# Performance work log

Measured on AMD Instinct MI355X. Metric: run time of the kernel, lower is better.

Reference implementation:

```python
import jax, jax.numpy as jnp
import numpy as np
from jax import lax

# Fixed dims from MSSMamba defaults
B_, L_, DM = 2, 8192, 256
NH, HP, NS = 4, 64, 8          # nheads, headdim, d_state
DIN = NH * HP                  # d_inner = 256
DPROJ = 2 * DIN + 2 * NS + NH  # 532


def setup_inputs() -> dict:
    key = jax.random.key(0)
    ks = jax.random.split(key, 16)
    f = lambda k, s, sc=1.0: jax.random.normal(k, s, jnp.float32) * sc
    inp = {
        'x_H': f(ks[0], (B_, L_, DM)),
        'x_V': f(ks[1], (B_, L_, DM)),
        'W_in_H': f(ks[2], (DM, 2 * DPROJ), 0.05),
        'W_in_V': f(ks[3], (DM, 2 * DPROJ), 0.05),
        'W_out_HF': f(ks[4], (DIN, DM), 0.05),
        'W_out_HB': f(ks[5], (DIN, DM), 0.05),
        'W_out_VF': f(ks[6], (DIN, DM), 0.05),
        'W_out_VB': f(ks[7], (DIN, DM), 0.05),
        'W_out': f(ks[8], (4 * DM, DM), 0.05),
    }
    for i, nm in enumerate(['HF', 'HB', 'VF', 'VB']):
        kd = jax.random.fold_in(ks[9], i)
        ka = jax.random.fold_in(ks[10], i)
        inp['dt_bias_' + nm] = f(kd, (NH,), 0.1)
        inp['A_log_' + nm] = jnp.log(jax.random.uniform(ka, (NH,), jnp.float32, 1.0, 16.0))
        inp['D_' + nm] = jnp.ones((NH,), jnp.float32)
    # per-batch permutation mapping vertical position -> horizontal position
    inp['v2h'] = jax.vmap(lambda k: jax.random.permutation(k, L_))(
        jax.random.split(ks[11], B_)).astype(jnp.int32)
    return inp


def _scan_dir(zxbcdt, dt_bias, A_log, D):
    # zxbcdt: [b, l, DPROJ] -> Mamba2-style selective scan, ngroups=1
    z = zxbcdt[..., :DIN].reshape(B_, L_, NH, HP)
    xBC = jax.nn.silu(zxbcdt[..., DIN:DIN + DIN + 2 * NS])
    x = xBC[..., :DIN].reshape(B_, L_, NH, HP)
    Bm = xBC[..., DIN:DIN + NS]      # [b, l, n]
    Cm = xBC[..., DIN + NS:]         # [b, l, n]
    dt = jax.nn.softplus(zxbcdt[..., -NH:] + dt_bias)  # [b, l, h]
    A = -jnp.exp(A_log)              # [h]
    dA = jnp.exp(dt * A)             # [b, l, h]
    dBx = jnp.einsum('blh,bln,blhp->blhpn', dt, Bm, x)  # [b,l,h,p,n]

    def step(state, inp):
        dA_t, dBx_t, C_t = inp
        state = dA_t[..., None, None] * state + dBx_t   # [b,h,p,n]
        y_t = jnp.einsum('bhpn,bn->bhp', state, C_t)
        return state, y_t

    init = jnp.zeros((B_, NH, HP, NS), dt.dtype)
    _, ys = lax.scan(step, init, (jnp.moveaxis(dA, 1, 0),
                                  jnp.moveaxis(dBx, 1, 0),
                                  jnp.moveaxis(Cm, 1, 0)))
    y = jnp.moveaxis(ys, 0, 1) + D[None, None, :, None] * x  # skip D*x
    y = y * jax.nn.silu(z)                                   # gate
    return y.reshape(B_, L_, DIN)


def reference(x_H, x_V, W_in_H, W_in_V,
              dt_bias_HF, dt_bias_HB, dt_bias_VF, dt_bias_VB,
              A_log_HF, A_log_HB, A_log_VF, A_log_VB,
              D_HF, D_HB, D_VF, D_VB,
              W_out_HF, W_out_HB, W_out_VF, W_out_VB,
              W_out, v2h):
    zx_HF, zx_HB = jnp.split(x_H @ W_in_H, 2, axis=-1)
    zx_VF, zx_VB = jnp.split(x_V @ W_in_V, 2, axis=-1)
    # note: source applies out_proj_HB to the HF branch (kept faithful)
    y_HF = _scan_dir(zx_HF, dt_bias_HF, A_log_HF, D_HF) @ W_out_HB
    y_HB = _scan_dir(zx_HB[:, ::-1], dt_bias_HB, A_log_HB, D_HB)[:, ::-1] @ W_out_HF
    y_VF = _scan_dir(zx_VF, dt_bias_VF, A_log_VF, D_VF) @ W_out_VB
    y_VB = _scan_dir(zx_VB[:, ::-1], dt_bias_VB, A_log_VB, D_VB)[:, ::-1] @ W_out_VF
    # remap vertical-ordered outputs to horizontal ordering (scatter by v2h)
    bidx = jnp.arange(B_)[:, None]
    y_VF = jnp.zeros_like(y_VF).at[bidx, v2h].set(y_VF)
    y_VB = jnp.zeros_like(y_VB).at[bidx, v2h].set(y_VB)
    cat = jnp.concatenate([y_HF, y_HB, y_VF, y_VB], axis=-1)  # [b, l, 4*d_model]
    return jax.nn.silu(cat) @ W_out
```

## Files before the change

kernel.cpp:

```cpp
#include <hip/hip_runtime.h>
#include <hip/hip_bf16.h>

#define B_N 2
#define L_N 8192
#define ROWS 16384
#define CHUNK 32
#define NCHUNK 256
#define GRP 16
#define NGRP 16
#define NPAD 1152

typedef __bf16 bf16x8 __attribute__((ext_vector_type(8)));
typedef float f32x4 __attribute__((ext_vector_type(4)));

__device__ __forceinline__ float siluf(float v) {
  return v * __builtin_amdgcn_rcpf(1.f + __expf(-v));
}
__device__ __forceinline__ float softplusf_(float v) {
  return fmaxf(v, 0.f) + log1pf(__expf(-fabsf(v)));
}
__device__ __forceinline__ unsigned short f2bf(float v) {
  union { __bf16 b; unsigned short u; } x;
  x.b = (__bf16)v;
  return x.u;
}
__device__ __forceinline__ float bf2f(unsigned short u) {
  union { unsigned u; float f; } x; x.u = ((unsigned)u) << 16;
  return x.f;
}

__device__ __forceinline__ void gload_lds16(const unsigned short* g, unsigned short* l) {
  __builtin_amdgcn_global_load_lds(
      (const __attribute__((address_space(1))) unsigned int*)g,
      (__attribute__((address_space(3))) unsigned int*)l, 16, 0, 0);
}

struct P4 { const float* p[4]; };
struct ScanConsts {
  const float* dt_bias[4];
  const float* A_log[4];
  const float* D[4];
};

__global__ __launch_bounds__(256) void k_prep(
    const float* __restrict__ xH, const float* __restrict__ xV,
    const float* __restrict__ WH, const float* __restrict__ WV,
    P4 ws, const float* __restrict__ W_out, const int* __restrict__ v2h, ScanConsts sc,
    unsigned short* __restrict__ xbf, float* __restrict__ dtv_arr, float* __restrict__ dA_arr,
    unsigned short* __restrict__ Wt_in, unsigned short* __restrict__ Wt_dirs,
    unsigned short* __restrict__ Wt_fin, int* __restrict__ inv) {
  __shared__ float xs[32][257];
  __shared__ float Wsm[8][260];
  int bid = blockIdx.x;
  int tid = threadIdx.x;
  if (bid < 1024) {
    const int mat = bid >> 9;
    const float* x = mat ? xV : xH;
    const float* W = mat ? WV : WH;
    const int r0 = (bid & 511) * 32;
    for (int i = tid; i < 2048; i += 256) {
      int c = i >> 8, k = i & 255;
      int sl = c >> 2, h = c & 3;
      Wsm[c][k] = W[(long)k * 1064 + sl * 532 + 528 + h];
    }
    for (int i = tid; i < 32 * 64; i += 256) {
      int rl = i >> 6, kq = (i & 63) * 4;
      float4 v = *(const float4*)(x + (long)(r0 + rl) * 256 + kq);
      xs[rl][kq + 0] = v.x; xs[rl][kq + 1] = v.y; xs[rl][kq + 2] = v.z; xs[rl][kq + 3] = v.w;
    }
    __syncthreads();
    for (int i = tid; i < 32 * 64; i += 256) {
      int rl = i >> 6, kq = (i & 63) * 4;
      ushort4 o;
      o.x = f2bf(xs[rl][kq + 0]);
      o.y = f2bf(xs[rl][kq + 1]);
      o.z = f2bf(xs[rl][kq + 2]);
      o.w = f2bf(xs[rl][kq + 3]);
      *(ushort4*)(xbf + (size_t)mat * ROWS * 256 + (long)(r0 + rl) * 256 + kq) = o;
    }
    const int rl = tid >> 3, c = tid & 7;
    float s = 0.f;
    #pragma unroll 8
    for (int k = 0; k < 256; ++k) s = fmaf(xs[rl][k], Wsm[c][k], s);
    const int sl = c >> 2, h = c & 3;
    const int dir = mat * 2 + sl;
    float dtv = softplusf_(s + sc.dt_bias[dir][h]);
    float dAv = __expf(dtv * (-__expf(sc.A_log[dir][h])));
    long o = ((long)dir * 4 + h) * ROWS + (r0 + rl);
    dtv_arr[o] = dtv;
    dA_arr[o] = dAv;
  } else if (bid < 3328) {
    int i = (bid - 1024) * 256 + tid;
    int z = i / (NPAD * 256);
    int rem = i - z * (NPAD * 256);
    int n = rem >> 8, k = rem & 255;
    const float* W = z ? WV : WH;
    int sl = n >= 544;
    int cc = n - (sl ? 544 : 0);
    float v = (cc < 532) ? W[(long)k * 1064 + sl * 532 + cc] : 0.f;
    Wt_in[i] = f2bf(v);
  } else if (bid < 4352) {
    int i = (bid - 3328) * 256 + tid;
    int d = i >> 16;
    int rem = i & 65535;
    int n = rem >> 8, k = rem & 255;
    Wt_dirs[i] = f2bf(ws.p[d][(long)k * 256 + n]);
  } else if (bid < 5376) {
    int i = (bid - 4352) * 256 + tid;
    int n = i >> 10, k = i & 1023;
    Wt_fin[i] = f2bf(W_out[(long)k * 256 + n]);
  } else {
    int m = (bid - 5376) * 256 + tid;
    if (m < ROWS) {
      int b = m >> 13;
      inv[b * L_N + v2h[m]] = m;
    }
  }
}

struct EpiIn {
  unsigned short* zraw;
  unsigned short* xraw;
  unsigned short* bc;
};

__global__ __launch_bounds__(256) void k_gemm_in(
    const unsigned short* __restrict__ Abase, const unsigned short* __restrict__ Btbase,
    EpiIn ep) {
  __shared__ unsigned short smem[16384];
  unsigned short* AsB = smem;
  unsigned short* BsB = smem + 8192;
  const int tid = threadIdx.x;
  const int lane = tid & 63;
  const int wid = tid >> 6;
  const int wm = wid & 1, wn = wid >> 1;
  const int q = lane >> 4, r = lane & 15;
  const int m0 = blockIdx.x * 128;
  const int n0 = blockIdx.y * 128;
  const int z = blockIdx.z;
  const unsigned short* A = Abase + (long)z * ROWS * 256;
  const unsigned short* Bt = Btbase + (long)z * NPAD * 256;

  int s_row[2], s_ch[2];
  #pragma unroll
  for (int i = 0; i < 2; ++i) {
    int idx = i * 256 + tid;
    s_row[i] = idx >> 2;
    s_ch[i] = (idx & 3) ^ ((s_row[i] >> 1) & 3);
  }

  f32x4 acc[4][4] = {};
  const int swr = (r >> 1) & 3;
  int cur = 0;

  #pragma unroll
  for (int i = 0; i < 2; ++i) {
    gload_lds16(A + (long)(m0 + s_row[i]) * 256 + s_ch[i] * 8,
                AsB + (size_t)(i * 256 + wid * 64) * 8);
    gload_lds16(Bt + (long)(n0 + s_row[i]) * 256 + s_ch[i] * 8,
                BsB + (size_t)(i * 256 + wid * 64) * 8);
  }
  __syncthreads();

  for (int kt8 = 0; kt8 < 8; ++kt8) {
    const int kt = kt8 * 32;
    if (kt8 < 7) {
      #pragma unroll
      for (int i = 0; i < 2; ++i) {
        gload_lds16(A + (long)(m0 + s_row[i]) * 256 + kt + 32 + s_ch[i] * 8,
                    AsB + (size_t)((cur ^ 1) * 4096 + (i * 256 + wid * 64) * 8));
        gload_lds16(Bt + (long)(n0 + s_row[i]) * 256 + kt + 32 + s_ch[i] * 8,
                    BsB + (size_t)((cur ^ 1) * 4096 + (i * 256 + wid * 64) * 8));
      }
    }
    bf16x8 af[4], bfr[4];
    #pragma unroll
    for (int mi = 0; mi < 4; ++mi)
      af[mi] = *(const bf16x8*)&AsB[cur * 4096 + ((wm * 64 + mi * 16 + r) * 4 + (q ^ swr)) * 8];
    #pragma unroll
    for (int ni = 0; ni < 4; ++ni)
      bfr[ni] = *(const bf16x8*)&BsB[cur * 4096 + ((wn * 64 + ni * 16 + r) * 4 + (q ^ swr)) * 8];
    __builtin_amdgcn_s_setprio(1);
    #pragma unroll
    for (int mi = 0; mi < 4; ++mi)
      #pragma unroll
      for (int ni = 0; ni < 4; ++ni)
        acc[mi][ni] = __builtin_amdgcn_mfma_f32_16x16x32_bf16(af[mi], bfr[ni], acc[mi][ni], 0, 0, 0);
    __builtin_amdgcn_s_setprio(0);
    __syncthreads();
    cur ^= 1;
  }

  unsigned short* tr = smem + wid * (16 * 72);
  #pragma unroll
  for (int mi = 0; mi < 4; ++mi) {
    #pragma unroll
    for (int ni = 0; ni < 4; ++ni)
      #pragma unroll
      for (int j = 0; j < 4; ++j)
        tr[(q * 4 + j) * 72 + ni * 16 + r] = f2bf(acc[mi][ni][j]);
    asm volatile("s_waitcnt lgkmcnt(0)" ::: "memory");
    #pragma unroll
    for (int pass = 0; pass < 2; ++pass) {
      int rl = pass * 8 + (lane >> 3);
      int c8 = (lane & 7) * 8;
      bf16x8 v = *(const bf16x8*)&tr[rl * 72 + c8];
      int row = m0 + wm * 64 + mi * 16 + rl;
      int col = n0 + wn * 64 + c8;
      int sl = col >= 544;
      int cc = col - (sl ? 544 : 0);
      if (cc < 528) {
        int dir = z * 2 + sl;
        if (cc < 256)
          *(bf16x8*)(ep.zraw + ((long)dir * ROWS + row) * 256 + cc) = v;
        else if (cc < 512)
          *(bf16x8*)(ep.xraw + ((long)dir * ROWS + row) * 256 + cc - 256) = v;
        else
          *(bf16x8*)(ep.bc + ((long)dir * ROWS + row) * 16 + cc - 512) = v;
      }
    }
    asm volatile("s_waitcnt lgkmcnt(0)" ::: "memory");
  }
}

__global__ __launch_bounds__(512, 4) void k_fuse(
    const unsigned short* __restrict__ ybf,
    const unsigned short* __restrict__ Wt_dirs,
    const unsigned short* __restrict__ Wt_fin,
    unsigned short* __restrict__ pbuf) {
  __shared__ unsigned short Ab[2][64 * 32];
  __shared__ unsigned short Bb[2][256 * 32];
  __shared__ unsigned short Tl[64 * 264];
  const int tid = threadIdx.x;
  const int lane = tid & 63;
  const int wid = tid >> 6;
  const int wm = wid & 1, wn = wid >> 1;
  const int q = lane >> 4, r = lane & 15;
  const int r0 = blockIdx.x * 64;
  const int pair = blockIdx.y;
  const int swr = (r >> 1) & 3;

  const int a_row = tid >> 2;
  const int a_ch = (tid & 3) ^ ((a_row >> 1) & 3);
  const long a_off = (long)(r0 + a_row) * 256 + a_ch * 8;
  int b_row[2], b_ch[2];
  #pragma unroll
  for (int rnd = 0; rnd < 2; ++rnd) {
    int idx = rnd * 512 + tid;
    b_row[rnd] = idx >> 2;
    b_ch[rnd] = (idx & 3) ^ ((b_row[rnd] >> 1) & 3);
  }

  f32x4 acc_o[2][4] = {};
  int cur = 0;

  {
    const unsigned short* yd = ybf + (long)(pair * 2) * ROWS * 256;
    const unsigned short* Wd = Wt_dirs + (long)(pair * 2) * 65536;
    if (tid < 256)
      gload_lds16(yd + a_off, &Ab[0][(size_t)(wid * 64) * 8]);
    #pragma unroll
    for (int rnd = 0; rnd < 2; ++rnd)
      gload_lds16(Wd + (long)b_row[rnd] * 256 + b_ch[rnd] * 8,
                  &Bb[0][(size_t)(rnd * 512 + wid * 64) * 8]);
  }
  __syncthreads();

  #pragma unroll
  for (int dd = 0; dd < 2; ++dd) {
    const int d = pair * 2 + dd;
    const unsigned short* yd = ybf + (long)d * ROWS * 256;
    const unsigned short* Wd = Wt_dirs + (long)d * 65536;

    f32x4 acc_t[2][4] = {};
    for (int kt8 = 0; kt8 < 8; ++kt8) {
      const int kt = kt8 * 32;
      if (kt8 < 7) {
        if (tid < 256)
          gload_lds16(yd + a_off + kt + 32, &Ab[cur ^ 1][(size_t)(wid * 64) * 8]);
        #pragma unroll
        for (int rnd = 0; rnd < 2; ++rnd)
          gload_lds16(Wd + (long)b_row[rnd] * 256 + kt + 32 + b_ch[rnd] * 8,
                      &Bb[cur ^ 1][(size_t)(rnd * 512 + wid * 64) * 8]);
      } else {
        #pragma unroll
        for (int rnd = 0; rnd < 2; ++rnd)
          gload_lds16(Wt_fin + (long)b_row[rnd] * 1024 + d * 256 + b_ch[rnd] * 8,
                      &Bb[cur ^ 1][(size_t)(rnd * 512 + wid * 64) * 8]);
      }
      bf16x8 af[2], bfr[4];
      #pragma unroll
      for (int mi = 0; mi < 2; ++mi)
        af[mi] = *(const bf16x8*)&Ab[cur][((wm * 32 + mi * 16 + r) * 4 + (q ^ swr)) * 8];
      #pragma unroll
      for (int ni = 0; ni < 4; ++ni)
        bfr[ni] = *(const bf16x8*)&Bb[cur][((wn * 64 + ni * 16 + r) * 4 + (q ^ swr)) * 8];
      __builtin_amdgcn_s_setprio(1);
      #pragma unroll
      for (int mi = 0; mi < 2; ++mi)
        #pragma unroll
        for (int ni = 0; ni < 4; ++ni)
          acc_t[mi][ni] = __builtin_amdgcn_mfma_f32_16x16x32_bf16(af[mi], bfr[ni], acc_t[mi][ni], 0, 0, 0);
      __builtin_amdgcn_s_setprio(0);
      __syncthreads();
      cur ^= 1;
    }
    #pragma unroll
    for (int mi = 0; mi < 2; ++mi)
      #pragma unroll
      for (int ni = 0; ni < 4; ++ni)
        #pragma unroll
        for (int j = 0; j < 4; ++j)
          Tl[(wm * 32 + mi * 16 + q * 4 + j) * 264 + wn * 64 + ni * 16 + r] =
              f2bf(siluf(acc_t[mi][ni][j]));
    __syncthreads();
    for (int kt8 = 0; kt8 < 8; ++kt8) {
      const int kt = kt8 * 32;
      if (kt8 < 7) {
        #pragma unroll
        for (int rnd = 0; rnd < 2; ++rnd)
          gload_lds16(Wt_fin + (long)b_row[rnd] * 1024 + d * 256 + kt + 32 + b_ch[rnd] * 8,
                      &Bb[cur ^ 1][(size_t)(rnd * 512 + wid * 64) * 8]);
      } else if (dd == 0) {
        const unsigned short* yd1 = ybf + (long)(d + 1) * ROWS * 256;
        const unsigned short* Wd1 = Wt_dirs + (long)(d + 1) * 65536;
        if (tid < 256)
          gload_lds16(yd1 + a_off, &Ab[cur ^ 1][(size_t)(wid * 64) * 8]);
        #pragma unroll
        for (int rnd = 0; rnd < 2; ++rnd)
          gload_lds16(Wd1 + (long)b_row[rnd] * 256 + b_ch[rnd] * 8,
                      &Bb[cur ^ 1][(size_t)(rnd * 512 + wid * 64) * 8]);
      }
      bf16x8 af[2], bfr[4];
      #pragma unroll
      for (int mi = 0; mi < 2; ++mi)
        af[mi] = *(const bf16x8*)&Tl[(wm * 32 + mi * 16 + r) * 264 + kt + q * 8];
      #pragma unroll
      for (int ni = 0; ni < 4; ++ni)
        bfr[ni] = *(const bf16x8*)&Bb[cur][((wn * 64 + ni * 16 + r) * 4 + (q ^ swr)) * 8];
      __builtin_amdgcn_s_setprio(1);
      #pragma unroll
      for (int mi = 0; mi < 2; ++mi)
        #pragma unroll
        for (int ni = 0; ni < 4; ++ni)
          acc_o[mi][ni] = __builtin_amdgcn_mfma_f32_16x16x32_bf16(af[mi], bfr[ni], acc_o[mi][ni], 0, 0, 0);
      __builtin_amdgcn_s_setprio(0);
      __syncthreads();
      cur ^= 1;
    }
  }

  #pragma unroll
  for (int mi = 0; mi < 2; ++mi)
    #pragma unroll
    for (int ni = 0; ni < 4; ++ni)
      #pragma unroll
      for (int j = 0; j < 4; ++j)
        Tl[(wm * 32 + mi * 16 + q * 4 + j) * 264 + wn * 64 + ni * 16 + r] = f2bf(acc_o[mi][ni][j]);
  __syncthreads();
  unsigned short* pout = pbuf + (long)pair * ROWS * 256;
  #pragma unroll
  for (int pass = 0; pass < 4; ++pass) {
    int id = pass * 512 + tid;
    int row = id >> 5, c8 = (id & 31) * 8;
    bf16x8 v = *(const bf16x8*)&Tl[row * 264 + c8];
    *(bf16x8*)(pout + (long)(r0 + row) * 256 + c8) = v;
  }
}

__global__ void k_red(const unsigned short* __restrict__ pbuf,
                      const int* __restrict__ inv, float* __restrict__ out) {
  int i = blockIdx.x * 256 + threadIdx.x;
  int row = i >> 5, c8 = (i & 31) * 8;
  uint4 a = *(const uint4*)(pbuf + (long)row * 256 + c8);
  int vrow = inv[row];
  uint4 b = *(const uint4*)(pbuf + (size_t)ROWS * 256 + (long)vrow * 256 + c8);
  const unsigned short* au = (const unsigned short*)&a;
  const unsigned short* bu = (const unsigned short*)&b;
  float rr[8];
  #pragma unroll
  for (int j = 0; j < 8; ++j) rr[j] = bf2f(au[j]) + bf2f(bu[j]);
  ((float4*)out)[i * 2] = *(float4*)&rr[0];
  ((float4*)out)[i * 2 + 1] = *(float4*)&rr[4];
}

struct ScanP {
  const unsigned short* xraw;
  const unsigned short* zraw;
  const unsigned short* bc;
  const float* dtv;
  const float* dA;
  const float* D[4];
};

__global__ __launch_bounds__(64) void k_scan1(ScanP sp, float* __restrict__ S,
                                              float* __restrict__ P) {
  __shared__ __align__(16) float Bst[CHUNK][8];
  __shared__ float dAs[CHUNK];
  const int p = threadIdx.x;
  const int c = blockIdx.x;
  const int bh = blockIdx.y;
  const int d = blockIdx.z;
  const int b = bh >> 2, h = bh & 3;
  const int rev = d & 1;
  const int t0 = c * CHUNK;
  if (p < CHUNK) {
    const int t = t0 + p;
    const int l = rev ? (L_N - 1 - t) : t;
    const int row = (b << 13) + l;
    uint4 bv = *(const uint4*)(sp.bc + ((long)d * ROWS + row) * 16);
    const unsigned short* bu = (const unsigned short*)&bv;
    float dtvv = sp.dtv[((long)d * 4 + h) * ROWS + row];
    dAs[p] = sp.dA[((long)d * 4 + h) * ROWS + row];
    #pragma unroll
    for (int n = 0; n < 8; ++n) Bst[p][n] = siluf(bf2f(bu[n])) * dtvv;
  }
  __syncthreads();

  float st[8] = {0, 0, 0, 0, 0, 0, 0, 0};
  float cumdA = 1.f;
  const int l0 = rev ? (L_N - 1 - t0) : t0;
  const unsigned short* xp = sp.xraw + ((long)d * ROWS + (b << 13) + l0) * 256 + h * 64 + p;
  const long stp = rev ? -256L : 256L;

  unsigned short xa[8], xb[8];
  #pragma unroll
  for (int j = 0; j < 8; ++j) xa[j] = xp[(long)j * stp];
  #pragma unroll
  for (int g = 0; g < 4; ++g) {
    if (g < 3) {
      #pragma unroll
      for (int j = 0; j < 8; ++j) xb[j] = xp[(long)((g + 1) * 8 + j) * stp];
    }
    #pragma unroll
    for (int j = 0; j < 8; ++j) {
      int s = g * 8 + j;
      float x = siluf(bf2f(xa[j]));
      float dA = dAs[s];
      f32x4 B0 = *(const f32x4*)&Bst[s][0];
      f32x4 B1 = *(const f32x4*)&Bst[s][4];
      cumdA *= dA;
      st[0] = fmaf(dA, st[0], x * B0[0]);
      st[1] = fmaf(dA, st[1], x * B0[1]);
      st[2] = fmaf(dA, st[2], x * B0[2]);
      st[3] = fmaf(dA, st[3], x * B0[3]);
      st[4] = fmaf(dA, st[4], x * B1[0]);
      st[5] = fmaf(dA, st[5], x * B1[1]);
      st[6] = fmaf(dA, st[6], x * B1[2]);
      st[7] = fmaf(dA, st[7], x * B1[3]);
    }
    #pragma unroll
    for (int j = 0; j < 8; ++j) xa[j] = xb[j];
  }
  float* Sp = S + ((((long)d * NCHUNK + c) * 8 + bh) * 64 + p) * 8;
  #pragma unroll
  for (int n = 0; n < 8; ++n) Sp[n] = st[n];
  if (p == 0) P[((long)d * NCHUNK + c) * 8 + bh] = cumdA;
}

__global__ __launch_bounds__(512) void k_scan2a(const float* __restrict__ S,
                                                const float* __restrict__ P,
                                                float* __restrict__ carry_loc,
                                                float* __restrict__ Sg,
                                                float* __restrict__ Pg) {
  __shared__ float Pl[GRP];
  const int tid = threadIdx.x;
  const int gid = blockIdx.x;
  const int g = gid & 15;
  const int dbh = gid >> 4;
  const int d = dbh >> 3, bh = dbh & 7;
  if (tid < GRP) Pl[tid] = P[((long)d * NCHUNK + g * GRP + tid) * 8 + bh];
  __syncthreads();
  float cy = 0.f;
  #pragma unroll
  for (int i = 0; i < GRP; ++i) {
    const int c = g * GRP + i;
    carry_loc[(((long)d * NCHUNK + c) * 8 + bh) * 512 + tid] = cy;
    const float Sv = S[(((long)d * NCHUNK + c) * 8 + bh) * 512 + tid];
    cy = fmaf(Pl[i], cy, Sv);
  }
  Sg[(((long)d * NGRP + g) * 8 + bh) * 512 + tid] = cy;
  if (tid == 0) {
    float pp = 1.f;
    #pragma unroll
    for (int i = 0; i < GRP; ++i) pp *= Pl[i];
    Pg[((long)d * NGRP + g) * 8 + bh] = pp;
  }
}

__global__ __launch_bounds__(512) void k_scan2b(const float* __restrict__ Sg,
                                                const float* __restrict__ Pg,
                                                float* __restrict__ gcarry) {
  __shared__ float Pgl[NGRP];
  const int tid = threadIdx.x;
  const int dbh = blockIdx.x;
  const int d = dbh >> 3, bh = dbh & 7;
  if (tid < NGRP) Pgl[tid] = Pg[((long)d * NGRP + tid) * 8 + bh];
  __syncthreads();
  float cy = 0.f;
  #pragma unroll
  for (int g = 0; g < NGRP; ++g) {
    gcarry[(((long)d * NGRP + g) * 8 + bh) * 512 + tid] = cy;
    const float Sv = Sg[(((long)d * NGRP + g) * 8 + bh) * 512 + tid];
    cy = fmaf(Pgl[g], cy, Sv);
  }
}

__global__ __launch_bounds__(64) void k_scan3(ScanP sp,
                                              const float* __restrict__ carry_loc,
                                              const float* __restrict__ gcarry,
                                              const float* __restrict__ Pc,
                                              unsigned short* __restrict__ ybf) {
  __shared__ __align__(16) float Bst[CHUNK][8];
  __shared__ __align__(16) float Cst[CHUNK][8];
  __shared__ float dAs[CHUNK];
  __shared__ float Pgr[GRP];
  const int p = threadIdx.x;
  const int c = blockIdx.x;
  const int bh = blockIdx.y;
  const int d = blockIdx.z;
  const int b = bh >> 2, h = bh & 3;
  const int rev = d & 1;
  const float Dv = sp.D[d][h];
  const int t0 = c * CHUNK;
  const int grp = c >> 4, ii = c & 15;
  if (p < ii) Pgr[p] = Pc[((long)d * NCHUNK + grp * GRP + p) * 8 + bh];
  if (p < CHUNK) {
    const int t = t0 + p;
    const int l = rev ? (L_N - 1 - t) : t;
    const int row = (b << 13) + l;
    const unsigned short* bp = sp.bc + ((long)d * ROWS + row) * 16;
    uint4 bv = *(const uint4*)bp;
    uint4 cv = *(const uint4*)(bp + 8);
    const unsigned short* bu = (const unsigned short*)&bv;
    const unsigned short* cu = (const unsigned short*)&cv;
    float dtvv = sp.dtv[((long)d * 4 + h) * ROWS + row];
    dAs[p] = sp.dA[((long)d * 4 + h) * ROWS + row];
    #pragma unroll
    for (int n = 0; n < 8; ++n) Bst[p][n] = siluf(bf2f(bu[n])) * dtvv;
    #pragma unroll
    for (int n = 0; n < 8; ++n) Cst[p][n] = siluf(bf2f(cu[n]));
  }
  __syncthreads();

  float pref = 1.f;
  for (int k = 0; k < ii; ++k) pref *= Pgr[k];
  float st[8];
  {
    const float* clp = carry_loc + ((((long)d * NCHUNK + c) * 8 + bh) * 64 + p) * 8;
    const float* gcp = gcarry + ((((long)d * NGRP + grp) * 8 + bh) * 64 + p) * 8;
    #pragma unroll
    for (int n = 0; n < 8; ++n) st[n] = fmaf(pref, gcp[n], clp[n]);
  }

  const int l0 = rev ? (L_N - 1 - t0) : t0;
  const long base = (long)(b << 13) + l0;
  const unsigned short* xp = sp.xraw + ((long)d * ROWS + base) * 256 + h * 64 + p;
  const unsigned short* zp = sp.zraw + ((long)d * ROWS + base) * 256 + h * 64 + p;
  unsigned short* yp = ybf + ((long)d * ROWS + base) * 256 + h * 64 + p;
  const long stp = rev ? -256L : 256L;

  unsigned short xa[8], xb[8], za[8], zb[8];
  #pragma unroll
  for (int j = 0; j < 8; ++j) { xa[j] = xp[(long)j * stp]; za[j] = zp[(long)j * stp]; }
  #pragma unroll
  for (int g = 0; g < 4; ++g) {
    if (g < 3) {
      #pragma unroll
      for (int j = 0; j < 8; ++j) {
        xb[j] = xp[(long)((g + 1) * 8 + j) * stp];
        zb[j] = zp[(long)((g + 1) * 8 + j) * stp];
      }
    }
    #pragma unroll
    for (int j = 0; j < 8; ++j) {
      int s = g * 8 + j;
      float x = siluf(bf2f(xa[j]));
      float zv = siluf(bf2f(za[j]));
      float dA = dAs[s];
      f32x4 B0 = *(const f32x4*)&Bst[s][0];
      f32x4 B1 = *(const f32x4*)&Bst[s][4];
      f32x4 C0 = *(const f32x4*)&Cst[s][0];
      f32x4 C1 = *(const f32x4*)&Cst[s][4];
      st[0] = fmaf(dA, st[0], x * B0[0]);
      st[1] = fmaf(dA, st[1], x * B0[1]);
      st[2] = fmaf(dA, st[2], x * B0[2]);
      st[3] = fmaf(dA, st[3], x * B0[3]);
      st[4] = fmaf(dA, st[4], x * B1[0]);
      st[5] = fmaf(dA, st[5], x * B1[1]);
      st[6] = fmaf(dA, st[6], x * B1[2]);
      st[7] = fmaf(dA, st[7], x * B1[3]);
      float y01 = fmaf(st[1], C0[1], st[0] * C0[0]);
      float y23 = fmaf(st[3], C0[3], st[2] * C0[2]);
      float y45 = fmaf(st[5], C1[1], st[4] * C1[0]);
      float y67 = fmaf(st[7], C1[3], st[6] * C1[2]);
      float y = (y01 + y23) + (y45 + y67);
      y = fmaf(Dv, x, y) * zv;
      yp[(long)s * stp] = f2bf(y);
    }
    #pragma unroll
    for (int j = 0; j < 8; ++j) { xa[j] = xb[j]; za[j] = zb[j]; }
  }
}

extern "C" void kernel_launch(void* const* d_in, const int* in_sizes, int n_in,
                              void* d_out, int out_size, void* d_ws, size_t ws_size,
                              hipStream_t stream) {
  const float* x_H = (const float*)d_in[0];
  const float* x_V = (const float*)d_in[1];
  const float* W_in_H = (const float*)d_in[2];
  const float* W_in_V = (const float*)d_in[3];
  const float* W_out_HF = (const float*)d_in[4];
  const float* W_out_HB = (const float*)d_in[5];
  const float* W_out_VF = (const float*)d_in[6];
  const float* W_out_VB = (const float*)d_in[7];
  const float* W_out = (const float*)d_in[8];
  const float* dt_bias_HF = (const float*)d_in[9];
  const float* A_log_HF = (const float*)d_in[10];
  const float* D_HF = (const float*)d_in[11];
  const float* dt_bias_HB = (const float*)d_in[12];
  const float* A_log_HB = (const float*)d_in[13];
  const float* D_HB = (const float*)d_in[14];
  const float* dt_bias_VF = (const float*)d_in[15];
  const float* A_log_VF = (const float*)d_in[16];
  const float* D_VF = (const float*)d_in[17];
  const float* dt_bias_VB = (const float*)d_in[18];
  const float* A_log_VB = (const float*)d_in[19];
  const float* D_VB = (const float*)d_in[20];
  const int* v2h = (const int*)d_in[21];

  char* ws = (char*)d_ws;
  size_t off = 0;
  auto alloc = [&](size_t bytes) {
    void* pp = ws + off;
    off = (off + bytes + 255) & ~(size_t)255;
    return pp;
  };
  unsigned short* xbf = (unsigned short*)alloc((size_t)2 * ROWS * 256 * 2);
  unsigned short* Wt_in = (unsigned short*)alloc((size_t)2 * NPAD * 256 * 2);
  unsigned short* Wt_dirs = (unsigned short*)alloc((size_t)4 * 65536 * 2);
  unsigned short* Wt_fin = (unsigned short*)alloc((size_t)256 * 1024 * 2);
  unsigned short* zraw = (unsigned short*)alloc((size_t)4 * ROWS * 256 * 2);
  unsigned short* xraw = (unsigned short*)alloc((size_t)4 * ROWS * 256 * 2);
  unsigned short* bc = (unsigned short*)alloc((size_t)4 * ROWS * 16 * 2);
  float* dtv_arr = (float*)alloc((size_t)16 * ROWS * 4);
  float* dA_arr = (float*)alloc((size_t)16 * ROWS * 4);
  unsigned short* ybf = (unsigned short*)alloc((size_t)4 * ROWS * 256 * 2);
  float* S = (float*)alloc((size_t)4 * NCHUNK * 8 * 512 * 4);
  float* P = (float*)alloc((size_t)4 * NCHUNK * 8 * 4);
  float* carry_loc = (float*)alloc((size_t)4 * NCHUNK * 8 * 512 * 4);
  float* Sg = (float*)alloc((size_t)4 * NGRP * 8 * 512 * 4);
  float* Pg = (float*)alloc((size_t)4 * NGRP * 8 * 4);
  float* gcarry = (float*)alloc((size_t)4 * NGRP * 8 * 512 * 4);
  int* inv = (int*)alloc((size_t)ROWS * 4);
  unsigned short* pbuf = (unsigned short*)alloc((size_t)2 * ROWS * 256 * 2);

  ScanConsts sc;
  sc.dt_bias[0] = dt_bias_HF; sc.dt_bias[1] = dt_bias_HB;
  sc.dt_bias[2] = dt_bias_VF; sc.dt_bias[3] = dt_bias_VB;
  sc.A_log[0] = A_log_HF; sc.A_log[1] = A_log_HB;
  sc.A_log[2] = A_log_VF; sc.A_log[3] = A_log_VB;
  sc.D[0] = D_HF; sc.D[1] = D_HB; sc.D[2] = D_VF; sc.D[3] = D_VB;

  P4 wdirs;
  wdirs.p[0] = W_out_HB; wdirs.p[1] = W_out_HF; wdirs.p[2] = W_out_VB; wdirs.p[3] = W_out_VF;

  k_prep<<<5440, 256, 0, stream>>>(x_H, x_V, W_in_H, W_in_V, wdirs, W_out, v2h, sc,
                                   xbf, dtv_arr, dA_arr, Wt_in, Wt_dirs, Wt_fin, inv);

  EpiIn ep; ep.zraw = zraw; ep.xraw = xraw; ep.bc = bc;

  k_gemm_in<<<dim3(ROWS / 128, NPAD / 128, 2), 256, 0, stream>>>(xbf, Wt_in, ep);

  ScanP sp;
  sp.xraw = xraw; sp.zraw = zraw; sp.bc = bc; sp.dtv = dtv_arr; sp.dA = dA_arr;
  sp.D[0] = D_HF; sp.D[1] = D_HB; sp.D[2] = D_VF; sp.D[3] = D_VB;

  k_scan1<<<dim3(NCHUNK, 8, 4), 64, 0, stream>>>(sp, S, P);
  k_scan2a<<<512, 512, 0, stream>>>(S, P, carry_loc, Sg, Pg);
  k_scan2b<<<32, 512, 0, stream>>>(Sg, Pg, gcarry);
  k_scan3<<<dim3(NCHUNK, 8, 4), 64, 0, stream>>>(sp, carry_loc, gcarry, P, ybf);

  k_fuse<<<dim3(ROWS / 64, 2), 512, 0, stream>>>(ybf, Wt_dirs, Wt_fin, pbuf);
  k_red<<<ROWS * 256 / 8 / 256, 256, 0, stream>>>(pbuf, inv, (float*)d_out);

  (void)in_sizes; (void)n_in; (void)out_size; (void)ws_size;
}
```

Baseline: 254.2 us.

## Triple-buffer LDS loads in input and fused output GEMMs with one barrier per step

Both the input-projection GEMM and the fused out-projection kernel move from double-buffered LDS with two syncthreads per k-step to a 3-slot ring buffer. Each step prefetches two tiles ahead and uses an explicit vmcnt wait plus a single s_barrier. The fused kernel flattens its four sub-GEMMs into one 32-step global tile schedule, so prefetch continues across the phase boundaries. This raises LDS use per block and drops the 4-blocks occupancy hint on k_fuse, which may reduce occupancy.

```diff
diff --git a/kernel.cpp b/kernel.cpp
--- a/kernel.cpp
+++ b/kernel.cpp
@@ -127,9 +127,7 @@
 __global__ __launch_bounds__(256) void k_gemm_in(
     const unsigned short* __restrict__ Abase, const unsigned short* __restrict__ Btbase,
     EpiIn ep) {
-  __shared__ unsigned short smem[16384];
-  unsigned short* AsB = smem;
-  unsigned short* BsB = smem + 8192;
+  __shared__ unsigned short smem[24576];
   const int tid = threadIdx.x;
   const int lane = tid & 63;
   const int wid = tid >> 6;
@@ -149,37 +147,41 @@
     s_ch[i] = (idx & 3) ^ ((s_row[i] >> 1) & 3);
   }
 
+  auto stage = [&](int ti) {
+    const int slot = ti % 3;
+    const int kt = ti * 32;
+    #pragma unroll
+    for (int i = 0; i < 2; ++i) {
+      gload_lds16(A + (long)(m0 + s_row[i]) * 256 + kt + s_ch[i] * 8,
+                  smem + (size_t)slot * 4096 + (size_t)(i * 256 + wid * 64) * 8);
+      gload_lds16(Bt + (long)(n0 + s_row[i]) * 256 + kt + s_ch[i] * 8,
+                  smem + 12288 + (size_t)slot * 4096 + (size_t)(i * 256 + wid * 64) * 8);
+    }
+  };
+
   f32x4 acc[4][4] = {};
   const int swr = (r >> 1) & 3;
-  int cur = 0;
-
-  #pragma unroll
-  for (int i = 0; i < 2; ++i) {
-    gload_lds16(A + (long)(m0 + s_row[i]) * 256 + s_ch[i] * 8,
-                AsB + (size_t)(i * 256 + wid * 64) * 8);
-    gload_lds16(Bt + (long)(n0 + s_row[i]) * 256 + s_ch[i] * 8,
-                BsB + (size_t)(i * 256 + wid * 64) * 8);
-  }
-  __syncthreads();
-
-  for (int kt8 = 0; kt8 < 8; ++kt8) {
-    const int kt = kt8 * 32;
-    if (kt8 < 7) {
-      #pragma unroll
-      for (int i = 0; i < 2; ++i) {
-        gload_lds16(A + (long)(m0 + s_row[i]) * 256 + kt + 32 + s_ch[i] * 8,
-                    AsB + (size_t)((cur ^ 1) * 4096 + (i * 256 + wid * 64) * 8));
-        gload_lds16(Bt + (long)(n0 + s_row[i]) * 256 + kt + 32 + s_ch[i] * 8,
-                    BsB + (size_t)((cur ^ 1) * 4096 + (i * 256 + wid * 64) * 8));
-      }
-    }
+
+  stage(0);
+  stage(1);
+
+  #pragma unroll
+  for (int i = 0; i < 8; ++i) {
+    if (i < 7) asm volatile("s_waitcnt vmcnt(4)" ::: "memory");
+    else       asm volatile("s_waitcnt vmcnt(0)" ::: "memory");
+    __builtin_amdgcn_s_barrier();
+    __builtin_amdgcn_sched_barrier(0);
+    if (i + 2 < 8) stage(i + 2);
+    const int slot = i % 3;
     bf16x8 af[4], bfr[4];
     #pragma unroll
     for (int mi = 0; mi < 4; ++mi)
-      af[mi] = *(const bf16x8*)&AsB[cur * 4096 + ((wm * 64 + mi * 16 + r) * 4 + (q ^ swr)) * 8];
+      af[mi] = *(const bf16x8*)&smem[(size_t)slot * 4096 +
+                                     ((wm * 64 + mi * 16 + r) * 4 + (q ^ swr)) * 8];
     #pragma unroll
     for (int ni = 0; ni < 4; ++ni)
-      bfr[ni] = *(const bf16x8*)&BsB[cur * 4096 + ((wn * 64 + ni * 16 + r) * 4 + (q ^ swr)) * 8];
+      bfr[ni] = *(const bf16x8*)&smem[12288 + (size_t)slot * 4096 +
+                                      ((wn * 64 + ni * 16 + r) * 4 + (q ^ swr)) * 8];
     __builtin_amdgcn_s_setprio(1);
     #pragma unroll
     for (int mi = 0; mi < 4; ++mi)
@@ -187,9 +189,8 @@
       for (int ni = 0; ni < 4; ++ni)
         acc[mi][ni] = __builtin_amdgcn_mfma_f32_16x16x32_bf16(af[mi], bfr[ni], acc[mi][ni], 0, 0, 0);
     __builtin_amdgcn_s_setprio(0);
-    __syncthreads();
-    cur ^= 1;
-  }
+  }
+  __syncthreads();
 
   unsigned short* tr = smem + wid * (16 * 72);
   #pragma unroll
@@ -223,14 +224,15 @@
   }
 }
 
-__global__ __launch_bounds__(512, 4) void k_fuse(
+__global__ __launch_bounds__(512) void k_fuse(
     const unsigned short* __restrict__ ybf,
     const unsigned short* __restrict__ Wt_dirs,
     const unsigned short* __restrict__ Wt_fin,
     unsigned short* __restrict__ pbuf) {
-  __shared__ unsigned short Ab[2][64 * 32];
-  __shared__ unsigned short Bb[2][256 * 32];
-  __shared__ unsigned short Tl[64 * 264];
+  __shared__ unsigned short smf[47616];
+  unsigned short* Ab = smf;
+  unsigned short* Bb = smf + 6144;
+  unsigned short* Tl = smf + 30720;
   const int tid = threadIdx.x;
   const int lane = tid & 63;
   const int wid = tid >> 6;
@@ -251,50 +253,51 @@
     b_ch[rnd] = (idx & 3) ^ ((b_row[rnd] >> 1) & 3);
   }
 
+  auto stageT = [&](int g) {
+    const int seg = g >> 3, ti = g & 7, kt = ti * 32;
+    const int dl = pair * 2 + (seg >> 1);
+    const int slot = g % 3;
+    if ((seg & 1) == 0) {
+      if (tid < 256)
+        gload_lds16(ybf + (long)dl * ROWS * 256 + a_off + kt,
+                    Ab + (size_t)slot * 2048 + (size_t)(wid * 64) * 8);
+      #pragma unroll
+      for (int rnd = 0; rnd < 2; ++rnd)
+        gload_lds16(Wt_dirs + (long)dl * 65536 + (long)b_row[rnd] * 256 + kt + b_ch[rnd] * 8,
+                    Bb + (size_t)slot * 8192 + (size_t)(rnd * 512 + wid * 64) * 8);
+    } else {
+      #pragma unroll
+      for (int rnd = 0; rnd < 2; ++rnd)
+        gload_lds16(Wt_fin + (long)b_row[rnd] * 1024 + dl * 256 + kt + b_ch[rnd] * 8,
+                    Bb + (size_t)slot * 8192 + (size_t)(rnd * 512 + wid * 64) * 8);
+    }
+  };
+
   f32x4 acc_o[2][4] = {};
-  int cur = 0;
-
-  {
-    const unsigned short* yd = ybf + (long)(pair * 2) * ROWS * 256;
-    const unsigned short* Wd = Wt_dirs + (long)(pair * 2) * 65536;
-    if (tid < 256)
-      gload_lds16(yd + a_off, &Ab[0][(size_t)(wid * 64) * 8]);
-    #pragma unroll
-    for (int rnd = 0; rnd < 2; ++rnd)
-      gload_lds16(Wd + (long)b_row[rnd] * 256 + b_ch[rnd] * 8,
-                  &Bb[0][(size_t)(rnd * 512 + wid * 64) * 8]);
-  }
-  __syncthreads();
+
+  stageT(0);
+  stageT(1);
 
   #pragma unroll
   for (int dd = 0; dd < 2; ++dd) {
-    const int d = pair * 2 + dd;
-    const unsigned short* yd = ybf + (long)d * ROWS * 256;
-    const unsigned short* Wd = Wt_dirs + (long)d * 65536;
-
     f32x4 acc_t[2][4] = {};
-    for (int kt8 = 0; kt8 < 8; ++kt8) {
-      const int kt = kt8 * 32;
-      if (kt8 < 7) {
-        if (tid < 256)
-          gload_lds16(yd + a_off + kt + 32, &Ab[cur ^ 1][(size_t)(wid * 64) * 8]);
-        #pragma unroll
-        for (int rnd = 0; rnd < 2; ++rnd)
-          gload_lds16(Wd + (long)b_row[rnd] * 256 + kt + 32 + b_ch[rnd] * 8,
-                      &Bb[cur ^ 1][(size_t)(rnd * 512 + wid * 64) * 8]);
-      } else {
-        #pragma unroll
-        for (int rnd = 0; rnd < 2; ++rnd)
-          gload_lds16(Wt_fin + (long)b_row[rnd] * 1024 + d * 256 + b_ch[rnd] * 8,
-                      &Bb[cur ^ 1][(size_t)(rnd * 512 + wid * 64) * 8]);
-      }
+    #pragma unroll
+    for (int i = 0; i < 8; ++i) {
+      const int g = dd * 16 + i;
+      asm volatile("s_waitcnt vmcnt(2)" ::: "memory");
+      __builtin_amdgcn_s_barrier();
+      __builtin_amdgcn_sched_barrier(0);
+      stageT(g + 2);
+      const int slot = g % 3;
       bf16x8 af[2], bfr[4];
       #pragma unroll
       for (int mi = 0; mi < 2; ++mi)
-        af[mi] = *(const bf16x8*)&Ab[cur][((wm * 32 + mi * 16 + r) * 4 + (q ^ swr)) * 8];
+        af[mi] = *(const bf16x8*)&Ab[(size_t)slot * 2048 +
+                                     ((wm * 32 + mi * 16 + r) * 4 + (q ^ swr)) * 8];
       #pragma unroll
       for (int ni = 0; ni < 4; ++ni)
-        bfr[ni] = *(const bf16x8*)&Bb[cur][((wn * 64 + ni * 16 + r) * 4 + (q ^ swr)) * 8];
+        bfr[ni] = *(const bf16x8*)&Bb[(size_t)slot * 8192 +
+                                      ((wn * 64 + ni * 16 + r) * 4 + (q ^ swr)) * 8];
       __builtin_amdgcn_s_setprio(1);
       #pragma unroll
       for (int mi = 0; mi < 2; ++mi)
@@ -302,8 +305,6 @@
         for (int ni = 0; ni < 4; ++ni)
           acc_t[mi][ni] = __builtin_amdgcn_mfma_f32_16x16x32_bf16(af[mi], bfr[ni], acc_t[mi][ni], 0, 0, 0);
       __builtin_amdgcn_s_setprio(0);
-      __syncthreads();
-      cur ^= 1;
     }
     #pragma unroll
     for (int mi = 0; mi < 2; ++mi)
@@ -313,31 +314,25 @@
         for (int j = 0; j < 4; ++j)
           Tl[(wm * 32 + mi * 16 + q * 4 + j) * 264 + wn * 64 + ni * 16 + r] =
               f2bf(siluf(acc_t[mi][ni][j]));
-    __syncthreads();
-    for (int kt8 = 0; kt8 < 8; ++kt8) {
-      const int kt = kt8 * 32;
-      if (kt8 < 7) {
-        #pragma unroll
-        for (int rnd = 0; rnd < 2; ++rnd)
-          gload_lds16(Wt_fin + (long)b_row[rnd] * 1024 + d * 256 + kt + 32 + b_ch[rnd] * 8,
-                      &Bb[cur ^ 1][(size_t)(rnd * 512 + wid * 64) * 8]);
-      } else if (dd == 0) {
-        const unsigned short* yd1 = ybf + (long)(d + 1) * ROWS * 256;
-        const unsigned short* Wd1 = Wt_dirs + (long)(d + 1) * 65536;
-        if (tid < 256)
-          gload_lds16(yd1 + a_off, &Ab[cur ^ 1][(size_t)(wid * 64) * 8]);
-        #pragma unroll
-        for (int rnd = 0; rnd < 2; ++rnd)
-          gload_lds16(Wd1 + (long)b_row[rnd] * 256 + b_ch[rnd] * 8,
-                      &Bb[cur ^ 1][(size_t)(rnd * 512 + wid * 64) * 8]);
-      }
+    asm volatile("s_waitcnt lgkmcnt(0)" ::: "memory");
+    #pragma unroll
+    for (int i = 0; i < 8; ++i) {
+      const int g = dd * 16 + 8 + i;
+      if (g < 31) asm volatile("s_waitcnt vmcnt(2)" ::: "memory");
+      else        asm volatile("s_waitcnt vmcnt(0)" ::: "memory");
+      __builtin_amdgcn_s_barrier();
+      __builtin_amdgcn_sched_barrier(0);
+      if (g + 2 < 32) stageT(g + 2);
+      const int slot = g % 3;
+      const int kt = i * 32;
       bf16x8 af[2], bfr[4];
       #pragma unroll
       for (int mi = 0; mi < 2; ++mi)
         af[mi] = *(const bf16x8*)&Tl[(wm * 32 + mi * 16 + r) * 264 + kt + q * 8];
       #pragma unroll
       for (int ni = 0; ni < 4; ++ni)
-        bfr[ni] = *(const bf16x8*)&Bb[cur][((wn * 64 + ni * 16 + r) * 4 + (q ^ swr)) * 8];
+        bfr[ni] = *(const bf16x8*)&Bb[(size_t)slot * 8192 +
+                                      ((wn * 64 + ni * 16 + r) * 4 + (q ^ swr)) * 8];
       __builtin_amdgcn_s_setprio(1);
       #pragma unroll
       for (int mi = 0; mi < 2; ++mi)
@@ -345,11 +340,10 @@
         for (int ni = 0; ni < 4; ++ni)
           acc_o[mi][ni] = __builtin_amdgcn_mfma_f32_16x16x32_bf16(af[mi], bfr[ni], acc_o[mi][ni], 0, 0, 0);
       __builtin_amdgcn_s_setprio(0);
-      __syncthreads();
-      cur ^= 1;
-    }
-  }
-
+    }
+  }
+
+  __syncthreads();
   #pragma unroll
   for (int mi = 0; mi < 2; ++mi)
     #pragma unroll
```

After: 251.6 us. Within noise of the previous version (-1.0%).
